# Kernel optimization log

Hardware: AMD Instinct MI355X
Metric: run time of the kernel (lower is better)

## Reference

```python
import jax, jax.numpy as jnp
import numpy as np

N = 4096          # num_nodes
K = 2             # max_diffusion_step
NUM_UNITS = 64
INPUT_DIM = 2
NNZ = 65536


def setup_inputs() -> dict:
    key = jax.random.key(0)
    ks = jax.random.split(key, 8)
    B = 64
    inputs = jax.random.normal(ks[0], (B, N * INPUT_DIM), dtype=jnp.float32)
    hx = jax.random.normal(ks[1], (B, N * NUM_UNITS), dtype=jnp.float32)
    sup_rows = jax.random.randint(ks[2], (2, NNZ), 0, N, dtype=jnp.int32)
    sup_cols = jax.random.randint(ks[3], (2, NNZ), 0, N, dtype=jnp.int32)
    sup_vals = jax.random.uniform(ks[4], (2, NNZ), dtype=jnp.float32)
    in_size = INPUT_DIM + NUM_UNITS           # 66
    num_mat = 2 * K + 1                        # 5
    W_ru = jax.random.normal(ks[5], (in_size * num_mat, 2 * NUM_UNITS), dtype=jnp.float32) * 0.05
    b_ru = jnp.ones((2 * NUM_UNITS,), dtype=jnp.float32)   # bias_start = 1.0
    W_c = jax.random.normal(ks[6], (in_size * num_mat, NUM_UNITS), dtype=jnp.float32) * 0.05
    b_c = jnp.zeros((NUM_UNITS,), dtype=jnp.float32)        # bias_start = 0.0
    return {"inputs": inputs, "hx": hx, "sup_rows": sup_rows, "sup_cols": sup_cols,
            "sup_vals": sup_vals, "W_ru": W_ru, "b_ru": b_ru, "W_c": W_c, "b_c": b_c}


def _spmm(rows, cols, vals, x):
    # sparse [N,N] @ dense [N,F] via gather + segment_sum
    return jax.ops.segment_sum(vals[:, None] * x[cols], rows, num_segments=N)


def _gconv(inputs, state, sup_rows, sup_cols, sup_vals, W, b):
    B = inputs.shape[0]
    x = jnp.concatenate([inputs.reshape(B, N, -1), state.reshape(B, N, -1)], axis=2)  # [B,N,F]
    F = x.shape[2]
    x0 = x.transpose(1, 2, 0).reshape(N, F * B)   # [N, F*B]
    xs = [x0]
    for s in range(2):  # two supports (dual random walk)
        r, c, v = sup_rows[s], sup_cols[s], sup_vals[s]
        x1 = _spmm(r, c, v, x0)
        xs.append(x1)
        xp, xpp = x1, x0
        for _ in range(2, K + 1):  # Chebyshev-style recurrence
            x2 = 2.0 * _spmm(r, c, v, xp) - xpp
            xs.append(x2)
            xp, xpp = x2, xp
    num_mat = len(xs)  # 2*K + 1
    xcat = jnp.stack(xs, axis=0).reshape(num_mat, N, F, B)
    xcat = xcat.transpose(3, 1, 2, 0).reshape(B * N, F * num_mat)  # [B*N, F*M]
    out = xcat @ W + b
    return out.reshape(B, N * W.shape[1])


def reference(inputs, hx, sup_rows, sup_cols, sup_vals, W_ru, b_ru, W_c, b_c):
    B = inputs.shape[0]
    value = jax.nn.sigmoid(_gconv(inputs, hx, sup_rows, sup_cols, sup_vals, W_ru, b_ru))
    value = value.reshape(B, N, 2 * NUM_UNITS)
    r = value[:, :, :NUM_UNITS].reshape(B, N * NUM_UNITS)
    u = value[:, :, NUM_UNITS:].reshape(B, N * NUM_UNITS)
    c = jnp.tanh(_gconv(inputs, r * hx, sup_rows, sup_cols, sup_vals, W_c, b_c))
    return u * hx + (1.0 - u) * c
```

## Files before the change

kernel.cpp:

```cpp
#include <hip/hip_runtime.h>

typedef float f32x4 __attribute__((ext_vector_type(4)));
typedef float f32x2 __attribute__((ext_vector_type(2)));
typedef short short8 __attribute__((ext_vector_type(8)));

#define NN 4096
#define HB 32
#define SROW 2048
#define IROW 64
#define SLVL 8388608ull
#define ILVL 262144ull
#define KP 352
#define KSTEPS 11
#define NPB 8

__device__ __forceinline__ ushort f2bf(float f){ uint i = __float_as_uint(f); return (ushort)((i + 0x7fffu + ((i >> 16) & 1u)) >> 16); }
__device__ __forceinline__ float bf2f(ushort u){ return __uint_as_float((uint)u << 16); }
__device__ __forceinline__ float lo_f(uint w){ return __uint_as_float(w << 16); }
__device__ __forceinline__ float hi_f(uint w){ return __uint_as_float(w & 0xffff0000u); }
__device__ __forceinline__ uint pkhi2(float a, float b){ return (uint)f2bf(a) | ((uint)f2bf(b) << 16); }
__device__ __forceinline__ float sigm(float x){ return 1.0f / (1.0f + __expf(-x)); }
__device__ __forceinline__ float tanh_fast(float x){
    x = fminf(20.0f, fmaxf(-20.0f, x));
    float t = __expf(-2.0f * x);
    return (1.0f - t) / (1.0f + t);
}
__device__ __forceinline__ f32x4 fma4(float v, f32x4 x, f32x4 a){
    a.x = fmaf(v, x.x, a.x); a.y = fmaf(v, x.y, a.y);
    a.z = fmaf(v, x.z, a.z); a.w = fmaf(v, x.w, a.w);
    return a;
}
__device__ __forceinline__ f32x4 fma4p(float v, uint2 u, f32x4 a){
    a.x = fmaf(v, lo_f(u.x), a.x); a.y = fmaf(v, hi_f(u.x), a.y);
    a.z = fmaf(v, lo_f(u.y), a.z); a.w = fmaf(v, hi_f(u.y), a.w);
    return a;
}

__global__ void zero_k(int* __restrict__ p){ p[blockIdx.x * 256 + threadIdx.x] = 0; }

__global__ void wtbuild_k(const float* __restrict__ Wru, const float* __restrict__ Wc,
                          ushort* __restrict__ ru_hi, ushort* __restrict__ ru_lo,
                          ushort* __restrict__ c_hi,  ushort* __restrict__ c_lo)
{
    int idx = blockIdx.x * 256 + threadIdx.x;
    float w = 0.0f;
    if (idx < 128 * KP) {
        int o = idx / KP, k = idx - o * KP;
        if (k < 330) { int m = k / 66, f = k - m * 66; w = Wru[(size_t)(f * 5 + m) * 128 + o]; }
        ushort hi = f2bf(w);
        ushort lo = f2bf(w - bf2f(hi));
        ru_hi[(size_t)o * KP + k] = hi;
        ru_lo[(size_t)o * KP + k] = lo;
    } else {
        int j = idx - 128 * KP;
        int o = j / KP, k = j - o * KP;
        if (k < 330) { int m = k / 66, f = k - m * 66; w = Wc[(size_t)(f * 5 + m) * 64 + o]; }
        ushort hi = f2bf(w);
        ushort lo = f2bf(w - bf2f(hi));
        c_hi[(size_t)o * KP + k] = hi;
        c_lo[(size_t)o * KP + k] = lo;
    }
}

__global__ void count_k(const int* __restrict__ rows, int* __restrict__ cnt)
{
    int i = blockIdx.x * 256 + threadIdx.x;
    int s = i >> 16;
    atomicAdd(&cnt[(s << 12) + rows[i]], 1);
}

__global__ __launch_bounds__(1024) void scan_k(const int* __restrict__ cnt, int* __restrict__ rp)
{
    int s = blockIdx.x;
    const int* c = cnt + (s << 12);
    int* r = rp + s * 4097;
    __shared__ int sd[1024];
    int tid = threadIdx.x;
    int i0 = tid * 4;
    int a0 = c[i0], a1 = c[i0 + 1], a2 = c[i0 + 2], a3 = c[i0 + 3];
    sd[tid] = a0 + a1 + a2 + a3;
    __syncthreads();
    for (int off = 1; off < 1024; off <<= 1) {
        int v = (tid >= off) ? sd[tid - off] : 0;
        __syncthreads();
        sd[tid] += v;
        __syncthreads();
    }
    int base = tid ? sd[tid - 1] : 0;
    r[i0] = base; r[i0 + 1] = base + a0; r[i0 + 2] = base + a0 + a1; r[i0 + 3] = base + a0 + a1 + a2;
    if (tid == 1023) r[4096] = sd[1023];
}

__global__ void scatter_k(const int* __restrict__ rows, const int* __restrict__ cols,
                          const float* __restrict__ vals, const int* __restrict__ rp,
                          int* __restrict__ fill, int2* __restrict__ pcv)
{
    int i = blockIdx.x * 256 + threadIdx.x;
    int s = i >> 16;
    int r = rows[i];
    int pos = rp[s * 4097 + r] + atomicAdd(&fill[(s << 12) + r], 1);
    int2 e; e.x = cols[i]; e.y = __float_as_int(vals[i]);
    pcv[(s << 16) + pos] = e;
}

__global__ void x0i_k(const float* __restrict__ in, float* __restrict__ x0i, int h)
{
    int i = blockIdx.x * 256 + threadIdx.x;
    int n = i >> 5, bl = i & 31;
    const f32x2 v = *(const f32x2*)(in + (size_t)(h * HB + bl) * 8192 + n * 2);
    *(f32x2*)(x0i + (size_t)n * IROW + bl * 2) = v;
}

template<int MODE>
__global__ __launch_bounds__(256) void spmm_k(
    const float* __restrict__ ss0, const float* __restrict__ si0,
    const float* __restrict__ ss1, const float* __restrict__ si1,
    float* __restrict__ ds0, float* __restrict__ di0,
    float* __restrict__ ds1, float* __restrict__ di1,
    const float* __restrict__ ps, const float* __restrict__ pi,
    const int* __restrict__ rp, const int2* __restrict__ pcv,
    int hxsm, int hxpm)
{
    const int b = blockIdx.x;
    const int tid = threadIdx.x;
    int s, sub = 0, rowgrp;
    bool is_main;
    if (MODE == 0) {
        s = blockIdx.y;
        if (b < 8192) {
            is_main = true;
            const int j = b >> 3;
            sub = (b & 7) * 2 + (j >> 9);
            rowgrp = j & 511;
        } else {
            is_main = false;
            rowgrp = b - 8192;
        }
    } else {
        if (b < 16384) {
            is_main = true;
            const int phase = b >> 12;
            s = phase >> 1;
            sub = (b & 7) * 2 + (phase & 1);
            rowgrp = (b >> 3) & 511;
        } else {
            is_main = false;
            const int j2 = b - 16384;
            s = j2 >> 8;
            rowgrp = j2 & 255;
        }
    }
    const int2* __restrict__ es = pcv + (s << 16);
    const int* __restrict__ rps = rp + s * 4097;
    const int wave = tid >> 6, lane = tid & 63;

    uint* dstu;
    const float* xf = nullptr;
    const uint*  xu = nullptr;
    const float* pb;
    int cshf = 0, cshu = 0, psh, r, gl, W, drow;
    if (is_main) {
        gl = lane & 31; W = 32;
        r = rowgrp * 8 + wave * 2 + ((lane >> 5) & 1);
        const int q = sub * 32 + gl;
        if (MODE == 0) {
            const float* xsrc = s ? ss1 : ss0;
            if (hxsm) { xf = xsrc + (size_t)(q >> 4) * 262144 + (q & 15) * 4; cshf = 6; }
            else      { xf = xsrc + q * 4;                                    cshf = 11; }
        } else {
            xu = (const uint*)(s ? ss1 : ss0) + q * 2; cshu = 10;
        }
        if (hxpm) { pb = ps + (size_t)(q >> 4) * 262144 + (q & 15) * 4; psh = 6; }
        else      { pb = ps + q * 4;                                    psh = 11; }
        dstu = (uint*)(s ? ds1 : ds0) + q * 2;
        drow = 1024;
    } else {
        gl = lane & 15; W = 16;
        r = rowgrp * 16 + wave * 4 + (lane >> 4);
        if (MODE == 0) { xf = (s ? si1 : si0) + gl * 4;               cshf = 6; }
        else           { xu = (const uint*)(s ? si1 : si0) + gl * 2;  cshu = 5; }
        pb = pi + gl * 4; psh = 6;
        dstu = (uint*)(s ? di1 : di0) + gl * 2;
        drow = 32;
    }
    const int pS = rps[r];
    const int cnt = rps[r + 1] - pS;

    f32x4 a0 = {0,0,0,0}, a1 = {0,0,0,0}, a2 = {0,0,0,0}, a3 = {0,0,0,0};
    for (int b2 = 0; b2 < cnt; b2 += W) {
        const int rem = cnt - b2;
        int2 E; E.x = 0; E.y = 0;
        if (gl < rem) E = es[pS + b2 + gl];
        const int n2 = rem < W ? rem : W;
        int j = 0;
        if (MODE == 0) {
            for (; j + 8 <= n2; j += 8) {
                const int c0 = __shfl(E.x, j + 0, W), c1 = __shfl(E.x, j + 1, W);
                const int c2 = __shfl(E.x, j + 2, W), c3 = __shfl(E.x, j + 3, W);
                const int c4 = __shfl(E.x, j + 4, W), c5 = __shfl(E.x, j + 5, W);
                const int c6 = __shfl(E.x, j + 6, W), c7 = __shfl(E.x, j + 7, W);
                const int v0 = __shfl(E.y, j + 0, W), v1 = __shfl(E.y, j + 1, W);
                const int v2 = __shfl(E.y, j + 2, W), v3 = __shfl(E.y, j + 3, W);
                const int v4 = __shfl(E.y, j + 4, W), v5 = __shfl(E.y, j + 5, W);
                const int v6 = __shfl(E.y, j + 6, W), v7 = __shfl(E.y, j + 7, W);
                const f32x4 x0v = *(const f32x4*)(xf + ((size_t)c0 << cshf));
                const f32x4 x1v = *(const f32x4*)(xf + ((size_t)c1 << cshf));
                const f32x4 x2v = *(const f32x4*)(xf + ((size_t)c2 << cshf));
                const f32x4 x3v = *(const f32x4*)(xf + ((size_t)c3 << cshf));
                const f32x4 x4v = *(const f32x4*)(xf + ((size_t)c4 << cshf));
                const f32x4 x5v = *(const f32x4*)(xf + ((size_t)c5 << cshf));
                const f32x4 x6v = *(const f32x4*)(xf + ((size_t)c6 << cshf));
                const f32x4 x7v = *(const f32x4*)(xf + ((size_t)c7 << cshf));
                a0 = fma4(__int_as_float(v0), x0v, a0);
                a1 = fma4(__int_as_float(v1), x1v, a1);
                a2 = fma4(__int_as_float(v2), x2v, a2);
                a3 = fma4(__int_as_float(v3), x3v, a3);
                a0 = fma4(__int_as_float(v4), x4v, a0);
                a1 = fma4(__int_as_float(v5), x5v, a1);
                a2 = fma4(__int_as_float(v6), x6v, a2);
                a3 = fma4(__int_as_float(v7), x7v, a3);
            }
            for (; j + 2 <= n2; j += 2) {
                const int c0 = __shfl(E.x, j, W), v0 = __shfl(E.y, j, W);
                const int c1 = __shfl(E.x, j + 1, W), v1 = __shfl(E.y, j + 1, W);
                const f32x4 x0v = *(const f32x4*)(xf + ((size_t)c0 << cshf));
                const f32x4 x1v = *(const f32x4*)(xf + ((size_t)c1 << cshf));
                a0 = fma4(__int_as_float(v0), x0v, a0);
                a1 = fma4(__int_as_float(v1), x1v, a1);
            }
            if (j < n2) {
                const int c0 = __shfl(E.x, j, W), v0 = __shfl(E.y, j, W);
                const f32x4 x0v = *(const f32x4*)(xf + ((size_t)c0 << cshf));
                a0 = fma4(__int_as_float(v0), x0v, a0);
            }
        } else {
            for (; j + 8 <= n2; j += 8) {
                const int c0 = __shfl(E.x, j + 0, W), c1 = __shfl(E.x, j + 1, W);
                const int c2 = __shfl(E.x, j + 2, W), c3 = __shfl(E.x, j + 3, W);
                const int c4 = __shfl(E.x, j + 4, W), c5 = __shfl(E.x, j + 5, W);
                const int c6 = __shfl(E.x, j + 6, W), c7 = __shfl(E.x, j + 7, W);
                const int v0 = __shfl(E.y, j + 0, W), v1 = __shfl(E.y, j + 1, W);
                const int v2 = __shfl(E.y, j + 2, W), v3 = __shfl(E.y, j + 3, W);
                const int v4 = __shfl(E.y, j + 4, W), v5 = __shfl(E.y, j + 5, W);
                const int v6 = __shfl(E.y, j + 6, W), v7 = __shfl(E.y, j + 7, W);
                const uint2 u0 = *(const uint2*)(xu + ((size_t)c0 << cshu));
                const uint2 u1 = *(const uint2*)(xu + ((size_t)c1 << cshu));
                const uint2 u2 = *(const uint2*)(xu + ((size_t)c2 << cshu));
                const uint2 u3 = *(const uint2*)(xu + ((size_t)c3 << cshu));
                const uint2 u4 = *(const uint2*)(xu + ((size_t)c4 << cshu));
                const uint2 u5 = *(const uint2*)(xu + ((size_t)c5 << cshu));
                const uint2 u6 = *(const uint2*)(xu + ((size_t)c6 << cshu));
                const uint2 u7 = *(const uint2*)(xu + ((size_t)c7 << cshu));
                a0 = fma4p(__int_as_float(v0), u0, a0);
                a1 = fma4p(__int_as_float(v1), u1, a1);
                a2 = fma4p(__int_as_float(v2), u2, a2);
                a3 = fma4p(__int_as_float(v3), u3, a3);
                a0 = fma4p(__int_as_float(v4), u4, a0);
                a1 = fma4p(__int_as_float(v5), u5, a1);
                a2 = fma4p(__int_as_float(v6), u6, a2);
                a3 = fma4p(__int_as_float(v7), u7, a3);
            }
            for (; j + 2 <= n2; j += 2) {
                const int c0 = __shfl(E.x, j, W), v0 = __shfl(E.y, j, W);
                const int c1 = __shfl(E.x, j + 1, W), v1 = __shfl(E.y, j + 1, W);
                const uint2 u0 = *(const uint2*)(xu + ((size_t)c0 << cshu));
                const uint2 u1 = *(const uint2*)(xu + ((size_t)c1 << cshu));
                a0 = fma4p(__int_as_float(v0), u0, a0);
                a1 = fma4p(__int_as_float(v1), u1, a1);
            }
            if (j < n2) {
                const int c0 = __shfl(E.x, j, W), v0 = __shfl(E.y, j, W);
                const uint2 u0 = *(const uint2*)(xu + ((size_t)c0 << cshu));
                a0 = fma4p(__int_as_float(v0), u0, a0);
            }
        }
    }
    f32x4 R;
    R.x = (a0.x + a1.x) + (a2.x + a3.x);
    R.y = (a0.y + a1.y) + (a2.y + a3.y);
    R.z = (a0.z + a1.z) + (a2.z + a3.z);
    R.w = (a0.w + a1.w) + (a2.w + a3.w);

    if (MODE) {
        const f32x4 pv = *(const f32x4*)(pb + ((size_t)r << psh));
        R.x = 2.0f * R.x - pv.x; R.y = 2.0f * R.y - pv.y;
        R.z = 2.0f * R.z - pv.z; R.w = 2.0f * R.w - pv.w;
    }
    uint2 o2;
    o2.x = pkhi2(R.x, R.y); o2.y = pkhi2(R.z, R.w);
    *(uint2*)(dstu + (size_t)r * drow) = o2;
}

template<int NT>
__device__ __forceinline__ void stage_hi(const float* __restrict__ xs, const float* __restrict__ xi,
                                         const float* __restrict__ m0s, int m0hx,
                                         int n, int tid, uint* __restrict__ Bhi)
{
    for (int i = tid; i < 480; i += NT) {
        int bl = i / 15, t = i - bl * 15;
        Bhi[bl * 180 + 165 + t] = 0u;
    }
    for (int i = tid; i < 2560; i += NT) {
        int m = i >> 9, rem = i & 511, bl = rem >> 4, fq = rem & 15;
        const int base = bl * 180 + m * 33 + 1 + fq * 2;
        if (m == 0) {
            const float* p = m0hx ? m0s + (size_t)bl * 262144 + (size_t)n * 64 + fq * 4
                                  : m0s + (size_t)n * SROW + bl * 64 + fq * 4;
            const f32x4 v = *(const f32x4*)p;
            Bhi[base]     = pkhi2(v.x, v.y);
            Bhi[base + 1] = pkhi2(v.z, v.w);
        } else {
            const uint* xp = (const uint*)(xs + (size_t)m * SLVL);
            const uint2 u = *(const uint2*)(xp + (size_t)n * 1024 + bl * 32 + fq * 2);
            Bhi[base]     = u.x;
            Bhi[base + 1] = u.y;
        }
    }
    for (int i = tid; i < 160; i += NT) {
        int m = i >> 5, bl = i & 31;
        if (m == 0) {
            const f32x2 v = *(const f32x2*)(xi + (size_t)n * IROW + bl * 2);
            Bhi[bl * 180] = pkhi2(v.x, v.y);
        } else {
            const uint* xp = (const uint*)(xi + (size_t)m * ILVL);
            Bhi[bl * 180 + m * 33] = xp[(size_t)n * 32 + bl];
        }
    }
}

#define MFMA(a, b, c) __builtin_amdgcn_mfma_f32_16x16x32_bf16(a, b, c, 0, 0, 0)

__global__ __launch_bounds__(512, 4) void mm_ru_k(const float* __restrict__ xs, const float* __restrict__ xi,
                                                  const ushort* __restrict__ whi, const ushort* __restrict__ wlo,
                                                  const float* __restrict__ bru, const float* __restrict__ hx,
                                                  float* __restrict__ uout, float* __restrict__ xs0s, int h)
{
    const int tid = threadIdx.x;
    const int lane = tid & 63, wave = tid >> 6;
    __shared__ uint Bbuf[2][5760];
    const int n0 = blockIdx.x * NPB;
    const float* hxs = hx + (size_t)h * HB * 262144;

    const int ob = wave * 16 + (lane & 15);
    const int ksub = (lane >> 4) * 8;
    const int brow = lane & 15;
    short8 Ah[KSTEPS], Al[KSTEPS];
    #pragma unroll
    for (int ks = 0; ks < KSTEPS; ++ks) {
        Ah[ks] = *(const short8*)(whi + (size_t)ob * KP + ks * 32 + ksub);
        Al[ks] = *(const short8*)(wlo + (size_t)ob * KP + ks * 32 + ksub);
    }
    const int g = lane >> 4, bcol = lane & 15;
    const int o = wave * 16 + g * 4;
    const float bb0 = bru[o], bb1 = bru[o + 1], bb2 = bru[o + 2], bb3 = bru[o + 3];

    stage_hi<512>(xs, xi, hxs, 1, n0, tid, Bbuf[0]);

    for (int i = 0; i < NPB; ++i) {
        __syncthreads();
        if (i + 1 < NPB)
            stage_hi<512>(xs, xi, hxs, 1, n0 + i + 1, tid, Bbuf[(i + 1) & 1]);
        const ushort* BH = (const ushort*)Bbuf[i & 1];
        const int n = n0 + i;
        f32x4 acc[2] = {};
        #pragma unroll
        for (int ks = 0; ks < KSTEPS; ++ks) {
            const int ko = ks * 32 + ksub;
            short8 Bh0 = *(const short8*)(BH + brow * 360 + ko);
            short8 Bh1 = *(const short8*)(BH + (16 + brow) * 360 + ko);
            acc[0] = MFMA(Ah[ks], Bh0, acc[0]);
            acc[1] = MFMA(Ah[ks], Bh1, acc[1]);
            acc[0] = MFMA(Al[ks], Bh0, acc[0]);
            acc[1] = MFMA(Al[ks], Bh1, acc[1]);
        }
        #pragma unroll
        for (int bt = 0; bt < 2; ++bt) {
            const int bl = bt * 16 + bcol;
            float s0 = sigm(acc[bt][0] + bb0);
            float s1 = sigm(acc[bt][1] + bb1);
            float s2 = sigm(acc[bt][2] + bb2);
            float s3 = sigm(acc[bt][3] + bb3);
            if (wave < 4) {
                const f32x4 hxv = *(const f32x4*)(hx + (size_t)(h * HB + bl) * 262144 + (size_t)n * 64 + o);
                f32x4 rv;
                rv[0] = s0 * hxv[0]; rv[1] = s1 * hxv[1];
                rv[2] = s2 * hxv[2]; rv[3] = s3 * hxv[3];
                *(f32x4*)(xs0s + (size_t)n * SROW + bl * 64 + o) = rv;
            } else {
                f32x4 uv = {s0, s1, s2, s3};
                *(f32x4*)(uout + (size_t)(h * HB + bl) * 262144 + (size_t)n * 64 + (o - 64)) = uv;
            }
        }
    }
}

__global__ __launch_bounds__(256, 4) void mm_c_k(const float* __restrict__ xs, const float* __restrict__ xi,
                                                 const ushort* __restrict__ whi, const ushort* __restrict__ wlo,
                                                 const float* __restrict__ bc, const float* __restrict__ hx,
                                                 float* __restrict__ out, int h)
{
    const int tid = threadIdx.x;
    const int lane = tid & 63, wave = tid >> 6;
    __shared__ uint Bbuf[2][5760];
    const int n0 = blockIdx.x * NPB;

    const int ob = wave * 16 + (lane & 15);
    const int ksub = (lane >> 4) * 8;
    const int brow = lane & 15;
    short8 Ah[KSTEPS], Al[KSTEPS];
    #pragma unroll
    for (int ks = 0; ks < KSTEPS; ++ks) {
        Ah[ks] = *(const short8*)(whi + (size_t)ob * KP + ks * 32 + ksub);
        Al[ks] = *(const short8*)(wlo + (size_t)ob * KP + ks * 32 + ksub);
    }
    const int g = lane >> 4, bcol = lane & 15;
    const int o = wave * 16 + g * 4;
    const float bb0 = bc[o], bb1 = bc[o + 1], bb2 = bc[o + 2], bb3 = bc[o + 3];

    stage_hi<256>(xs, xi, xs, 0, n0, tid, Bbuf[0]);

    for (int i = 0; i < NPB; ++i) {
        __syncthreads();
        if (i + 1 < NPB)
            stage_hi<256>(xs, xi, xs, 0, n0 + i + 1, tid, Bbuf[(i + 1) & 1]);
        const ushort* BH = (const ushort*)Bbuf[i & 1];
        const int n = n0 + i;
        f32x4 acc[2] = {};
        #pragma unroll
        for (int ks = 0; ks < KSTEPS; ++ks) {
            const int ko = ks * 32 + ksub;
            short8 Bh0 = *(const short8*)(BH + brow * 360 + ko);
            short8 Bh1 = *(const short8*)(BH + (16 + brow) * 360 + ko);
            acc[0] = MFMA(Ah[ks], Bh0, acc[0]);
            acc[1] = MFMA(Ah[ks], Bh1, acc[1]);
            acc[0] = MFMA(Al[ks], Bh0, acc[0]);
            acc[1] = MFMA(Al[ks], Bh1, acc[1]);
        }
        #pragma unroll
        for (int bt = 0; bt < 2; ++bt) {
            const int bl = bt * 16 + bcol;
            float c0 = tanh_fast(acc[bt][0] + bb0);
            float c1 = tanh_fast(acc[bt][1] + bb1);
            float c2 = tanh_fast(acc[bt][2] + bb2);
            float c3 = tanh_fast(acc[bt][3] + bb3);
            float* p = out + (size_t)(h * HB + bl) * 262144 + (size_t)n * 64 + o;
            const f32x4 hxv = *(const f32x4*)(hx + (size_t)(h * HB + bl) * 262144 + (size_t)n * 64 + o);
            f32x4 uv = *(const f32x4*)p;
            f32x4 ov;
            ov[0] = uv[0] * hxv[0] + (1.0f - uv[0]) * c0;
            ov[1] = uv[1] * hxv[1] + (1.0f - uv[1]) * c1;
            ov[2] = uv[2] * hxv[2] + (1.0f - uv[2]) * c2;
            ov[3] = uv[3] * hxv[3] + (1.0f - uv[3]) * c3;
            *(f32x4*)p = ov;
        }
    }
}

extern "C" void kernel_launch(void* const* d_in, const int* in_sizes, int n_in,
                              void* d_out, int out_size, void* d_ws, size_t ws_size,
                              hipStream_t stream)
{
    (void)in_sizes; (void)n_in; (void)out_size; (void)ws_size;
    const float* inputs  = (const float*)d_in[0];
    const float* hx      = (const float*)d_in[1];
    const int*   sup_rows= (const int*)d_in[2];
    const int*   sup_cols= (const int*)d_in[3];
    const float* sup_vals= (const float*)d_in[4];
    const float* W_ru    = (const float*)d_in[5];
    const float* b_ru    = (const float*)d_in[6];
    const float* W_c     = (const float*)d_in[7];
    const float* b_c     = (const float*)d_in[8];
    float* out = (float*)d_out;

    char* ws = (char*)d_ws;
    float* xs = (float*)ws;
    float* xi = xs + 5ull * SLVL;
    size_t off = (5ull * SLVL + 5ull * ILVL) * 4ull;
    ushort* wru_hi = (ushort*)(ws + off); off += 90112;
    ushort* wru_lo = (ushort*)(ws + off); off += 90112;
    ushort* wc_hi  = (ushort*)(ws + off); off += 45056;
    ushort* wc_lo  = (ushort*)(ws + off); off += 45056;
    int* row_ptr   = (int*)(ws + off);    off += 32800;
    int* cntfill   = (int*)(ws + off);    off += 65536;
    int2* pcv      = (int2*)(ws + off);   off += 1048576;

    #define XS(m) (xs + (size_t)(m) * SLVL)
    #define XI(m) (xi + (size_t)(m) * ILVL)
    int* fill = cntfill + 8192;

    zero_k<<<64, 256, 0, stream>>>(cntfill);
    wtbuild_k<<<264, 256, 0, stream>>>(W_ru, W_c, wru_hi, wru_lo, wc_hi, wc_lo);
    count_k<<<512, 256, 0, stream>>>(sup_rows, cntfill);
    scan_k<<<2, 1024, 0, stream>>>(cntfill, row_ptr);
    scatter_k<<<512, 256, 0, stream>>>(sup_rows, sup_cols, sup_vals, row_ptr, fill, pcv);

    for (int h = 0; h < 2; ++h) {
        const float* hxs = hx + (size_t)h * HB * 262144;
        x0i_k<<<512, 256, 0, stream>>>(inputs, XI(0), h);
        spmm_k<0><<<dim3(8448, 2), 256, 0, stream>>>(hxs, XI(0), hxs, XI(0),
                                                     XS(1), XI(1), XS(3), XI(3),
                                                     hxs, XI(0), row_ptr, pcv, 1, 0);
        spmm_k<1><<<dim3(16896, 1), 256, 0, stream>>>(XS(1), XI(1), XS(3), XI(3),
                                                      XS(2), XI(2), XS(4), XI(4),
                                                      hxs, XI(0), row_ptr, pcv, 0, 1);
        mm_ru_k<<<NN / NPB, 512, 0, stream>>>(xs, xi, wru_hi, wru_lo, b_ru, hx, out, XS(0), h);
        spmm_k<0><<<dim3(8448, 2), 256, 0, stream>>>(XS(0), XI(0), XS(0), XI(0),
                                                     XS(1), XI(1), XS(3), XI(3),
                                                     XS(0), XI(0), row_ptr, pcv, 0, 0);
        spmm_k<1><<<dim3(16896, 1), 256, 0, stream>>>(XS(1), XI(1), XS(3), XI(3),
                                                      XS(2), XI(2), XS(4), XI(4),
                                                      XS(0), XI(0), row_ptr, pcv, 0, 0);
        mm_c_k<<<NN / NPB, 256, 0, stream>>>(xs, xi, wc_hi, wc_lo, b_c, hx, out, h);
    }
    #undef XS
    #undef XI
}
```

Measured before the change: 700.5 us.

## Process both diffusion supports in one spmm thread to share source and prev loads

Each spmm thread now computes the row result for both supports at once, interleaving the two edge lists in the 8-wide gather loop, and launches half as many blocks. In MODE 0 both supports gather from the same source, so the two gather streams hit the same source tensor and can share cache locality. The Chebyshev previous-term value is loaded once and used for both outputs. This raises ILP and cuts block and index overhead, at the cost of more registers (two accumulator sets) and possible divergence when row degrees differ between supports.

```diff
diff --git a/kernel.cpp b/kernel.cpp
--- a/kernel.cpp
+++ b/kernel.cpp
@@ -111,6 +111,102 @@
     *(f32x2*)(x0i + (size_t)n * IROW + bl * 2) = v;
 }
 
+__device__ __forceinline__ void grp8f(int2 E, int j, int W, const float* __restrict__ xf, int cshf,
+                                      f32x4& a0, f32x4& a1, f32x4& a2, f32x4& a3)
+{
+    const int c0 = __shfl(E.x, j + 0, W), c1 = __shfl(E.x, j + 1, W);
+    const int c2 = __shfl(E.x, j + 2, W), c3 = __shfl(E.x, j + 3, W);
+    const int c4 = __shfl(E.x, j + 4, W), c5 = __shfl(E.x, j + 5, W);
+    const int c6 = __shfl(E.x, j + 6, W), c7 = __shfl(E.x, j + 7, W);
+    const int v0 = __shfl(E.y, j + 0, W), v1 = __shfl(E.y, j + 1, W);
+    const int v2 = __shfl(E.y, j + 2, W), v3 = __shfl(E.y, j + 3, W);
+    const int v4 = __shfl(E.y, j + 4, W), v5 = __shfl(E.y, j + 5, W);
+    const int v6 = __shfl(E.y, j + 6, W), v7 = __shfl(E.y, j + 7, W);
+    const f32x4 x0v = *(const f32x4*)(xf + ((size_t)c0 << cshf));
+    const f32x4 x1v = *(const f32x4*)(xf + ((size_t)c1 << cshf));
+    const f32x4 x2v = *(const f32x4*)(xf + ((size_t)c2 << cshf));
+    const f32x4 x3v = *(const f32x4*)(xf + ((size_t)c3 << cshf));
+    const f32x4 x4v = *(const f32x4*)(xf + ((size_t)c4 << cshf));
+    const f32x4 x5v = *(const f32x4*)(xf + ((size_t)c5 << cshf));
+    const f32x4 x6v = *(const f32x4*)(xf + ((size_t)c6 << cshf));
+    const f32x4 x7v = *(const f32x4*)(xf + ((size_t)c7 << cshf));
+    a0 = fma4(__int_as_float(v0), x0v, a0);
+    a1 = fma4(__int_as_float(v1), x1v, a1);
+    a2 = fma4(__int_as_float(v2), x2v, a2);
+    a3 = fma4(__int_as_float(v3), x3v, a3);
+    a0 = fma4(__int_as_float(v4), x4v, a0);
+    a1 = fma4(__int_as_float(v5), x5v, a1);
+    a2 = fma4(__int_as_float(v6), x6v, a2);
+    a3 = fma4(__int_as_float(v7), x7v, a3);
+}
+
+__device__ __forceinline__ void tailf(int2 E, int j, int n, int W, const float* __restrict__ xf, int cshf,
+                                      f32x4& a0, f32x4& a1, f32x4& a2, f32x4& a3)
+{
+    for (; j + 8 <= n; j += 8) grp8f(E, j, W, xf, cshf, a0, a1, a2, a3);
+    for (; j + 2 <= n; j += 2) {
+        const int c0 = __shfl(E.x, j, W), v0 = __shfl(E.y, j, W);
+        const int c1 = __shfl(E.x, j + 1, W), v1 = __shfl(E.y, j + 1, W);
+        const f32x4 x0v = *(const f32x4*)(xf + ((size_t)c0 << cshf));
+        const f32x4 x1v = *(const f32x4*)(xf + ((size_t)c1 << cshf));
+        a0 = fma4(__int_as_float(v0), x0v, a0);
+        a1 = fma4(__int_as_float(v1), x1v, a1);
+    }
+    if (j < n) {
+        const int c0 = __shfl(E.x, j, W), v0 = __shfl(E.y, j, W);
+        const f32x4 x0v = *(const f32x4*)(xf + ((size_t)c0 << cshf));
+        a0 = fma4(__int_as_float(v0), x0v, a0);
+    }
+}
+
+__device__ __forceinline__ void grp8p(int2 E, int j, int W, const uint* __restrict__ xu, int cshu,
+                                      f32x4& a0, f32x4& a1, f32x4& a2, f32x4& a3)
+{
+    const int c0 = __shfl(E.x, j + 0, W), c1 = __shfl(E.x, j + 1, W);
+    const int c2 = __shfl(E.x, j + 2, W), c3 = __shfl(E.x, j + 3, W);
+    const int c4 = __shfl(E.x, j + 4, W), c5 = __shfl(E.x, j + 5, W);
+    const int c6 = __shfl(E.x, j + 6, W), c7 = __shfl(E.x, j + 7, W);
+    const int v0 = __shfl(E.y, j + 0, W), v1 = __shfl(E.y, j + 1, W);
+    const int v2 = __shfl(E.y, j + 2, W), v3 = __shfl(E.y, j + 3, W);
+    const int v4 = __shfl(E.y, j + 4, W), v5 = __shfl(E.y, j + 5, W);
+    const int v6 = __shfl(E.y, j + 6, W), v7 = __shfl(E.y, j + 7, W);
+    const uint2 u0 = *(const uint2*)(xu + ((size_t)c0 << cshu));
+    const uint2 u1 = *(const uint2*)(xu + ((size_t)c1 << cshu));
+    const uint2 u2 = *(const uint2*)(xu + ((size_t)c2 << cshu));
+    const uint2 u3 = *(const uint2*)(xu + ((size_t)c3 << cshu));
+    const uint2 u4 = *(const uint2*)(xu + ((size_t)c4 << cshu));
+    const uint2 u5 = *(const uint2*)(xu + ((size_t)c5 << cshu));
+    const uint2 u6 = *(const uint2*)(xu + ((size_t)c6 << cshu));
+    const uint2 u7 = *(const uint2*)(xu + ((size_t)c7 << cshu));
+    a0 = fma4p(__int_as_float(v0), u0, a0);
+    a1 = fma4p(__int_as_float(v1), u1, a1);
+    a2 = fma4p(__int_as_float(v2), u2, a2);
+    a3 = fma4p(__int_as_float(v3), u3, a3);
+    a0 = fma4p(__int_as_float(v4), u4, a0);
+    a1 = fma4p(__int_as_float(v5), u5, a1);
+    a2 = fma4p(__int_as_float(v6), u6, a2);
+    a3 = fma4p(__int_as_float(v7), u7, a3);
+}
+
+__device__ __forceinline__ void tailp(int2 E, int j, int n, int W, const uint* __restrict__ xu, int cshu,
+                                      f32x4& a0, f32x4& a1, f32x4& a2, f32x4& a3)
+{
+    for (; j + 8 <= n; j += 8) grp8p(E, j, W, xu, cshu, a0, a1, a2, a3);
+    for (; j + 2 <= n; j += 2) {
+        const int c0 = __shfl(E.x, j, W), v0 = __shfl(E.y, j, W);
+        const int c1 = __shfl(E.x, j + 1, W), v1 = __shfl(E.y, j + 1, W);
+        const uint2 u0 = *(const uint2*)(xu + ((size_t)c0 << cshu));
+        const uint2 u1 = *(const uint2*)(xu + ((size_t)c1 << cshu));
+        a0 = fma4p(__int_as_float(v0), u0, a0);
+        a1 = fma4p(__int_as_float(v1), u1, a1);
+    }
+    if (j < n) {
+        const int c0 = __shfl(E.x, j, W), v0 = __shfl(E.y, j, W);
+        const uint2 u0 = *(const uint2*)(xu + ((size_t)c0 << cshu));
+        a0 = fma4p(__int_as_float(v0), u0, a0);
+    }
+}
+
 template<int MODE>
 __global__ __launch_bounds__(256) void spmm_k(
     const float* __restrict__ ss0, const float* __restrict__ si0,
@@ -123,172 +219,125 @@
 {
     const int b = blockIdx.x;
     const int tid = threadIdx.x;
-    int s, sub = 0, rowgrp;
-    bool is_main;
-    if (MODE == 0) {
-        s = blockIdx.y;
-        if (b < 8192) {
-            is_main = true;
-            const int j = b >> 3;
-            sub = (b & 7) * 2 + (j >> 9);
-            rowgrp = j & 511;
-        } else {
-            is_main = false;
-            rowgrp = b - 8192;
-        }
+    int sub = 0, rowgrp;
+    const bool is_main = b < 8192;
+    if (is_main) {
+        const int j = b >> 3;
+        sub = (b & 7) * 2 + (j >> 9);
+        rowgrp = j & 511;
     } else {
-        if (b < 16384) {
-            is_main = true;
-            const int phase = b >> 12;
-            s = phase >> 1;
-            sub = (b & 7) * 2 + (phase & 1);
-            rowgrp = (b >> 3) & 511;
-        } else {
-            is_main = false;
-            const int j2 = b - 16384;
-            s = j2 >> 8;
-            rowgrp = j2 & 255;
-        }
-    }
-    const int2* __restrict__ es = pcv + (s << 16);
-    const int* __restrict__ rps = rp + s * 4097;
-    const int wave = tid >> 6, lane = tid & 63;
-
-    uint* dstu;
-    const float* xf = nullptr;
-    const uint*  xu = nullptr;
-    const float* pb;
-    int cshf = 0, cshu = 0, psh, r, gl, W, drow;
+        rowgrp = b - 8192;
+    }
+    const int lane = tid & 63;
+    const int wave = tid >> 6;
+
+    const float* xf0 = nullptr;
+    const uint*  xu0 = nullptr;
+    const uint*  xu1 = nullptr;
+    const float* pb = nullptr;
+    uint *d0u, *d1u;
+    int cshf = 0, cshu = 0, psh = 0, r, gl, W, drow;
     if (is_main) {
         gl = lane & 31; W = 32;
         r = rowgrp * 8 + wave * 2 + ((lane >> 5) & 1);
         const int q = sub * 32 + gl;
         if (MODE == 0) {
-            const float* xsrc = s ? ss1 : ss0;
-            if (hxsm) { xf = xsrc + (size_t)(q >> 4) * 262144 + (q & 15) * 4; cshf = 6; }
-            else      { xf = xsrc + q * 4;                                    cshf = 11; }
+            if (hxsm) { xf0 = ss0 + (size_t)(q >> 4) * 262144 + (q & 15) * 4; cshf = 6; }
+            else      { xf0 = ss0 + q * 4;                                    cshf = 11; }
         } else {
-            xu = (const uint*)(s ? ss1 : ss0) + q * 2; cshu = 10;
-        }
-        if (hxpm) { pb = ps + (size_t)(q >> 4) * 262144 + (q & 15) * 4; psh = 6; }
-        else      { pb = ps + q * 4;                                    psh = 11; }
-        dstu = (uint*)(s ? ds1 : ds0) + q * 2;
+            xu0 = (const uint*)ss0 + q * 2;
+            xu1 = (const uint*)ss1 + q * 2; cshu = 10;
+            if (hxpm) { pb = ps + (size_t)(q >> 4) * 262144 + (q & 15) * 4; psh = 6; }
+            else      { pb = ps + q * 4;                                    psh = 11; }
+        }
+        d0u = (uint*)ds0 + q * 2;
+        d1u = (uint*)ds1 + q * 2;
         drow = 1024;
     } else {
         gl = lane & 15; W = 16;
         r = rowgrp * 16 + wave * 4 + (lane >> 4);
-        if (MODE == 0) { xf = (s ? si1 : si0) + gl * 4;               cshf = 6; }
-        else           { xu = (const uint*)(s ? si1 : si0) + gl * 2;  cshu = 5; }
-        pb = pi + gl * 4; psh = 6;
-        dstu = (uint*)(s ? di1 : di0) + gl * 2;
+        if (MODE == 0) { xf0 = si0 + gl * 4; cshf = 6; }
+        else {
+            xu0 = (const uint*)si0 + gl * 2;
+            xu1 = (const uint*)si1 + gl * 2; cshu = 5;
+            pb = pi + gl * 4; psh = 6;
+        }
+        d0u = (uint*)di0 + gl * 2;
+        d1u = (uint*)di1 + gl * 2;
         drow = 32;
     }
-    const int pS = rps[r];
-    const int cnt = rps[r + 1] - pS;
-
-    f32x4 a0 = {0,0,0,0}, a1 = {0,0,0,0}, a2 = {0,0,0,0}, a3 = {0,0,0,0};
-    for (int b2 = 0; b2 < cnt; b2 += W) {
-        const int rem = cnt - b2;
-        int2 E; E.x = 0; E.y = 0;
-        if (gl < rem) E = es[pS + b2 + gl];
-        const int n2 = rem < W ? rem : W;
+    const int pS0 = rp[r];        const int cnt0 = rp[r + 1] - pS0;
+    const int pS1 = rp[4097 + r]; const int cnt1 = rp[4097 + r + 1] - pS1;
+    const int2* __restrict__ es0 = pcv;
+    const int2* __restrict__ es1 = pcv + 65536;
+
+    f32x4 A0 = {0,0,0,0}, A1 = {0,0,0,0}, A2 = {0,0,0,0}, A3 = {0,0,0,0};
+    f32x4 B0 = {0,0,0,0}, B1 = {0,0,0,0}, B2 = {0,0,0,0}, B3 = {0,0,0,0};
+
+    if (cnt0 <= W && cnt1 <= W) {
+        int2 E0; E0.x = 0; E0.y = 0;
+        int2 E1; E1.x = 0; E1.y = 0;
+        if (gl < cnt0) E0 = es0[pS0 + gl];
+        if (gl < cnt1) E1 = es1[pS1 + gl];
+        const int f0 = cnt0 >> 3, f1 = cnt1 >> 3;
+        const int fm = (f0 < f1 ? f0 : f1) * 8;
         int j = 0;
         if (MODE == 0) {
-            for (; j + 8 <= n2; j += 8) {
-                const int c0 = __shfl(E.x, j + 0, W), c1 = __shfl(E.x, j + 1, W);
-                const int c2 = __shfl(E.x, j + 2, W), c3 = __shfl(E.x, j + 3, W);
-                const int c4 = __shfl(E.x, j + 4, W), c5 = __shfl(E.x, j + 5, W);
-                const int c6 = __shfl(E.x, j + 6, W), c7 = __shfl(E.x, j + 7, W);
-                const int v0 = __shfl(E.y, j + 0, W), v1 = __shfl(E.y, j + 1, W);
-                const int v2 = __shfl(E.y, j + 2, W), v3 = __shfl(E.y, j + 3, W);
-                const int v4 = __shfl(E.y, j + 4, W), v5 = __shfl(E.y, j + 5, W);
-                const int v6 = __shfl(E.y, j + 6, W), v7 = __shfl(E.y, j + 7, W);
-                const f32x4 x0v = *(const f32x4*)(xf + ((size_t)c0 << cshf));
-                const f32x4 x1v = *(const f32x4*)(xf + ((size_t)c1 << cshf));
-                const f32x4 x2v = *(const f32x4*)(xf + ((size_t)c2 << cshf));
-                const f32x4 x3v = *(const f32x4*)(xf + ((size_t)c3 << cshf));
-                const f32x4 x4v = *(const f32x4*)(xf + ((size_t)c4 << cshf));
-                const f32x4 x5v = *(const f32x4*)(xf + ((size_t)c5 << cshf));
-                const f32x4 x6v = *(const f32x4*)(xf + ((size_t)c6 << cshf));
-                const f32x4 x7v = *(const f32x4*)(xf + ((size_t)c7 << cshf));
-                a0 = fma4(__int_as_float(v0), x0v, a0);
-                a1 = fma4(__int_as_float(v1), x1v, a1);
-                a2 = fma4(__int_as_float(v2), x2v, a2);
-                a3 = fma4(__int_as_float(v3), x3v, a3);
-                a0 = fma4(__int_as_float(v4), x4v, a0);
-                a1 = fma4(__int_as_float(v5), x5v, a1);
-                a2 = fma4(__int_as_float(v6), x6v, a2);
-                a3 = fma4(__int_as_float(v7), x7v, a3);
+            for (; j < fm; j += 8) {
+                grp8f(E0, j, W, xf0, cshf, A0, A1, A2, A3);
+                grp8f(E1, j, W, xf0, cshf, B0, B1, B2, B3);
             }
-            for (; j + 2 <= n2; j += 2) {
-                const int c0 = __shfl(E.x, j, W), v0 = __shfl(E.y, j, W);
-                const int c1 = __shfl(E.x, j + 1, W), v1 = __shfl(E.y, j + 1, W);
-                const f32x4 x0v = *(const f32x4*)(xf + ((size_t)c0 << cshf));
-                const f32x4 x1v = *(const f32x4*)(xf + ((size_t)c1 << cshf));
-                a0 = fma4(__int_as_float(v0), x0v, a0);
-                a1 = fma4(__int_as_float(v1), x1v, a1);
+            tailf(E0, j, cnt0, W, xf0, cshf, A0, A1, A2, A3);
+            tailf(E1, j, cnt1, W, xf0, cshf, B0, B1, B2, B3);
+        } else {
+            for (; j < fm; j += 8) {
+                grp8p(E0, j, W, xu0, cshu, A0, A1, A2, A3);
+                grp8p(E1, j, W, xu1, cshu, B0, B1, B2, B3);
             }
-            if (j < n2) {
-                const int c0 = __shfl(E.x, j, W), v0 = __shfl(E.y, j, W);
-                const f32x4 x0v = *(const f32x4*)(xf + ((size_t)c0 << cshf));
-                a0 = fma4(__int_as_float(v0), x0v, a0);
-            }
-        } else {
-            for (; j + 8 <= n2; j += 8) {
-                const int c0 = __shfl(E.x, j + 0, W), c1 = __shfl(E.x, j + 1, W);
-                const int c2 = __shfl(E.x, j + 2, W), c3 = __shfl(E.x, j + 3, W);
-                const int c4 = __shfl(E.x, j + 4, W), c5 = __shfl(E.x, j + 5, W);
-                const int c6 = __shfl(E.x, j + 6, W), c7 = __shfl(E.x, j + 7, W);
-                const int v0 = __shfl(E.y, j + 0, W), v1 = __shfl(E.y, j + 1, W);
-                const int v2 = __shfl(E.y, j + 2, W), v3 = __shfl(E.y, j + 3, W);
-                const int v4 = __shfl(E.y, j + 4, W), v5 = __shfl(E.y, j + 5, W);
-                const int v6 = __shfl(E.y, j + 6, W), v7 = __shfl(E.y, j + 7, W);
-                const uint2 u0 = *(const uint2*)(xu + ((size_t)c0 << cshu));
-                const uint2 u1 = *(const uint2*)(xu + ((size_t)c1 << cshu));
-                const uint2 u2 = *(const uint2*)(xu + ((size_t)c2 << cshu));
-                const uint2 u3 = *(const uint2*)(xu + ((size_t)c3 << cshu));
-                const uint2 u4 = *(const uint2*)(xu + ((size_t)c4 << cshu));
-                const uint2 u5 = *(const uint2*)(xu + ((size_t)c5 << cshu));
-                const uint2 u6 = *(const uint2*)(xu + ((size_t)c6 << cshu));
-                const uint2 u7 = *(const uint2*)(xu + ((size_t)c7 << cshu));
-                a0 = fma4p(__int_as_float(v0), u0, a0);
-                a1 = fma4p(__int_as_float(v1), u1, a1);
-                a2 = fma4p(__int_as_float(v2), u2, a2);
-                a3 = fma4p(__int_as_float(v3), u3, a3);
-                a0 = fma4p(__int_as_float(v4), u4, a0);
-                a1 = fma4p(__int_as_float(v5), u5, a1);
-                a2 = fma4p(__int_as_float(v6), u6, a2);
-                a3 = fma4p(__int_as_float(v7), u7, a3);
-            }
-            for (; j + 2 <= n2; j += 2) {
-                const int c0 = __shfl(E.x, j, W), v0 = __shfl(E.y, j, W);
-                const int c1 = __shfl(E.x, j + 1, W), v1 = __shfl(E.y, j + 1, W);
-                const uint2 u0 = *(const uint2*)(xu + ((size_t)c0 << cshu));
-                const uint2 u1 = *(const uint2*)(xu + ((size_t)c1 << cshu));
-                a0 = fma4p(__int_as_float(v0), u0, a0);
-                a1 = fma4p(__int_as_float(v1), u1, a1);
-            }
-            if (j < n2) {
-                const int c0 = __shfl(E.x, j, W), v0 = __shfl(E.y, j, W);
-                const uint2 u0 = *(const uint2*)(xu + ((size_t)c0 << cshu));
-                a0 = fma4p(__int_as_float(v0), u0, a0);
-            }
-        }
-    }
-    f32x4 R;
-    R.x = (a0.x + a1.x) + (a2.x + a3.x);
-    R.y = (a0.y + a1.y) + (a2.y + a3.y);
-    R.z = (a0.z + a1.z) + (a2.z + a3.z);
-    R.w = (a0.w + a1.w) + (a2.w + a3.w);
+            tailp(E0, j, cnt0, W, xu0, cshu, A0, A1, A2, A3);
+            tailp(E1, j, cnt1, W, xu1, cshu, B0, B1, B2, B3);
+        }
+    } else {
+        for (int b2 = 0; b2 < cnt0; b2 += W) {
+            const int rem = cnt0 - b2;
+            int2 E; E.x = 0; E.y = 0;
+            if (gl < rem) E = es0[pS0 + b2 + gl];
+            const int n2 = rem < W ? rem : W;
+            if (MODE == 0) tailf(E, 0, n2, W, xf0, cshf, A0, A1, A2, A3);
+            else           tailp(E, 0, n2, W, xu0, cshu, A0, A1, A2, A3);
+        }
+        for (int b2 = 0; b2 < cnt1; b2 += W) {
+            const int rem = cnt1 - b2;
+            int2 E; E.x = 0; E.y = 0;
+            if (gl < rem) E = es1[pS1 + b2 + gl];
+            const int n2 = rem < W ? rem : W;
+            if (MODE == 0) tailf(E, 0, n2, W, xf0, cshf, B0, B1, B2, B3);
+            else           tailp(E, 0, n2, W, xu1, cshu, B0, B1, B2, B3);
+        }
+    }
+
+    f32x4 R0, R1;
+    R0.x = (A0.x + A1.x) + (A2.x + A3.x);
+    R0.y = (A0.y + A1.y) + (A2.y + A3.y);
+    R0.z = (A0.z + A1.z) + (A2.z + A3.z);
+    R0.w = (A0.w + A1.w) + (A2.w + A3.w);
+    R1.x = (B0.x + B1.x) + (B2.x + B3.x);
+    R1.y = (B0.y + B1.y) + (B2.y + B3.y);
+    R1.z = (B0.z + B1.z) + (B2.z + B3.z);
+    R1.w = (B0.w + B1.w) + (B2.w + B3.w);
 
     if (MODE) {
         const f32x4 pv = *(const f32x4*)(pb + ((size_t)r << psh));
-        R.x = 2.0f * R.x - pv.x; R.y = 2.0f * R.y - pv.y;
-        R.z = 2.0f * R.z - pv.z; R.w = 2.0f * R.w - pv.w;
-    }
-    uint2 o2;
-    o2.x = pkhi2(R.x, R.y); o2.y = pkhi2(R.z, R.w);
-    *(uint2*)(dstu + (size_t)r * drow) = o2;
+        R0.x = 2.0f * R0.x - pv.x; R0.y = 2.0f * R0.y - pv.y;
+        R0.z = 2.0f * R0.z - pv.z; R0.w = 2.0f * R0.w - pv.w;
+        R1.x = 2.0f * R1.x - pv.x; R1.y = 2.0f * R1.y - pv.y;
+        R1.z = 2.0f * R1.z - pv.z; R1.w = 2.0f * R1.w - pv.w;
+    }
+    uint2 o0, o1;
+    o0.x = pkhi2(R0.x, R0.y); o0.y = pkhi2(R0.z, R0.w);
+    o1.x = pkhi2(R1.x, R1.y); o1.y = pkhi2(R1.z, R1.w);
+    *(uint2*)(d0u + (size_t)r * drow) = o0;
+    *(uint2*)(d1u + (size_t)r * drow) = o1;
 }
 
 template<int NT>
@@ -497,19 +546,19 @@
     for (int h = 0; h < 2; ++h) {
         const float* hxs = hx + (size_t)h * HB * 262144;
         x0i_k<<<512, 256, 0, stream>>>(inputs, XI(0), h);
-        spmm_k<0><<<dim3(8448, 2), 256, 0, stream>>>(hxs, XI(0), hxs, XI(0),
-                                                     XS(1), XI(1), XS(3), XI(3),
-                                                     hxs, XI(0), row_ptr, pcv, 1, 0);
-        spmm_k<1><<<dim3(16896, 1), 256, 0, stream>>>(XS(1), XI(1), XS(3), XI(3),
-                                                      XS(2), XI(2), XS(4), XI(4),
-                                                      hxs, XI(0), row_ptr, pcv, 0, 1);
+        spmm_k<0><<<8448, 256, 0, stream>>>(hxs, XI(0), hxs, XI(0),
+                                            XS(1), XI(1), XS(3), XI(3),
+                                            hxs, XI(0), row_ptr, pcv, 1, 0);
+        spmm_k<1><<<8448, 256, 0, stream>>>(XS(1), XI(1), XS(3), XI(3),
+                                            XS(2), XI(2), XS(4), XI(4),
+                                            hxs, XI(0), row_ptr, pcv, 0, 1);
         mm_ru_k<<<NN / NPB, 512, 0, stream>>>(xs, xi, wru_hi, wru_lo, b_ru, hx, out, XS(0), h);
-        spmm_k<0><<<dim3(8448, 2), 256, 0, stream>>>(XS(0), XI(0), XS(0), XI(0),
-                                                     XS(1), XI(1), XS(3), XI(3),
-                                                     XS(0), XI(0), row_ptr, pcv, 0, 0);
-        spmm_k<1><<<dim3(16896, 1), 256, 0, stream>>>(XS(1), XI(1), XS(3), XI(3),
-                                                      XS(2), XI(2), XS(4), XI(4),
-                                                      XS(0), XI(0), row_ptr, pcv, 0, 0);
+        spmm_k<0><<<8448, 256, 0, stream>>>(XS(0), XI(0), XS(0), XI(0),
+                                            XS(1), XI(1), XS(3), XI(3),
+                                            XS(0), XI(0), row_ptr, pcv, 0, 0);
+        spmm_k<1><<<8448, 256, 0, stream>>>(XS(1), XI(1), XS(3), XI(3),
+                                            XS(2), XI(2), XS(4), XI(4),
+                                            XS(0), XI(0), row_ptr, pcv, 0, 0);
         mm_c_k<<<NN / NPB, 256, 0, stream>>>(xs, xi, wc_hi, wc_lo, b_c, hx, out, h);
     }
     #undef XS
```

Result: slower. 799.1 us (+14.1%).
